# Kernel optimization log

Hardware: AMD Instinct MI355X
Metric: run time of the kernel (lower is better)

Reference implementation:

```python
import jax, jax.numpy as jnp
from jax import lax
import numpy as np

RADIUS = 0.05
N_SEEDS = 40

def _farthest_point_sample(xyz, npoint):
    # xyz: [B, N, 3] -> seed indices [B, npoint]
    B, N, _ = xyz.shape
    dist0 = jnp.full((B, N), 1e10, dtype=xyz.dtype)
    far0 = jnp.zeros((B,), dtype=jnp.int32)  # deterministic init (torch uses randint)
    batch_idx = jnp.arange(B)

    def step(carry, _):
        distance, farthest = carry
        centroid = xyz[batch_idx, farthest][:, None, :]          # [B,1,3]
        d = jnp.sum((xyz - centroid) ** 2, axis=-1)              # [B,N]
        distance = jnp.minimum(distance, d)
        new_far = jnp.argmax(distance, axis=-1).astype(jnp.int32)
        return (distance, new_far), farthest

    _, cents = lax.scan(step, (dist0, far0), None, length=npoint)
    return cents.T                                               # [B, npoint]

def setup_inputs() -> dict:
    key = jax.random.key(0)
    pcs = jax.random.uniform(key, (16, 65536, 3), dtype=jnp.float32)
    return {"pcs": pcs}

def reference(pcs) -> jnp.ndarray:
    B, N, C = pcs.shape
    S = N_SEEDS
    seeds = _farthest_point_sample(pcs, S)                       # [B,S] int
    new_xyz = pcs[jnp.arange(B)[:, None], seeds]                 # [B,S,3]
    # squared pairwise distances seeds->points: [B,S,N]
    sqrdists = (jnp.sum(new_xyz ** 2, -1)[:, :, None]
                + jnp.sum(pcs ** 2, -1)[:, None, :]
                - 2.0 * jnp.einsum('bsc,bnc->bsn', new_xyz, pcs))
    relu_dists = jax.nn.relu(RADIUS ** 2 - sqrdists)
    den_mat = jnp.sum(relu_dists, axis=2)                        # [B,S]
    den_var = jnp.var(den_mat, axis=1, ddof=1).mean()            # torch.var is unbiased
    return den_var
```

## Files before the change

kernel.cpp:

```cpp
#include <hip/hip_runtime.h>

typedef unsigned long long ull;

#define NB    16
#define NPTS  65536
#define NSEED 40
#define BPB   16
#define TPB   1024
#define NW    16
#define PPT   4
#define R2    0.0025f
#define PAYLOAD 0xFFFFFFFFFFFFull
#define DONEG 40ull

__device__ __forceinline__ ull packdi(float v, int idx) {
  return ((ull)__float_as_uint(v) << 16) | (ull)((unsigned)(idx ^ 0xFFFF) & 0xFFFFu);
}

__global__ __launch_bounds__(TPB, 4) void fps_den_kernel(
    const float* __restrict__ pcs, ull* __restrict__ slots,
    ull* __restrict__ pden, float* __restrict__ out)
{
  const int beta = blockIdx.x >> 4;
  const int blk  = blockIdx.x & 15;
  const int tid  = threadIdx.x;
  const int lane = tid & 63;
  const int wav  = tid >> 6;
  const float* __restrict__ base = pcs + (size_t)beta * (NPTS * 3);

  __shared__ ull   sRedP[2][NW];
  __shared__ float sRedX[2][NW], sRedY[2][NW], sRedZ[2][NW];
  __shared__ float sWx[2], sWy[2], sWz[2];
  __shared__ float sSx[NSEED], sSy[NSEED], sSz[NSEED];
  __shared__ float sDen[NW][NSEED];
  __shared__ float sV[NB];

  float px[PPT], py[PPT], pz[PPT], dist[PPT];
#pragma unroll
  for (int j = 0; j < PPT; ++j) {
    int n = blk * (TPB * PPT) + j * TPB + tid;
    px[j] = base[n * 3 + 0];
    py[j] = base[n * 3 + 1];
    pz[j] = base[n * 3 + 2];
    dist[j] = 1e10f;
  }

  float cx = base[0], cy = base[1], cz = base[2];
  if (tid == 0) { sSx[0] = cx; sSy[0] = cy; sSz[0] = cz; }

  ull* myslots = slots + (size_t)beta * (2 * BPB * 4);

  for (int k = 0; k < NSEED - 1; ++k) {
    ull bestp = 0; float bx = 0.f, by = 0.f, bz = 0.f;
#pragma unroll
    for (int j = 0; j < PPT; ++j) {
      float dx = px[j] - cx, dy = py[j] - cy, dz = pz[j] - cz;
      float d  = __fadd_rn(__fadd_rn(__fmul_rn(dx, dx), __fmul_rn(dy, dy)),
                           __fmul_rn(dz, dz));
      float nd = fminf(dist[j], d);
      dist[j]  = nd;
      int n    = blk * (TPB * PPT) + j * TPB + tid;
      ull p    = packdi(nd, n);
      if (p > bestp) { bestp = p; bx = px[j]; by = py[j]; bz = pz[j]; }
    }
    ull mx = bestp;
#pragma unroll
    for (int o = 32; o > 0; o >>= 1) {
      ull q = __shfl_xor(mx, o, 64);
      mx = mx > q ? mx : q;
    }
    ull bal = __ballot(bestp == mx);
    int src = __ffsll((long long)bal) - 1;
    float gx = __shfl(bx, src, 64);
    float gy = __shfl(by, src, 64);
    float gz = __shfl(bz, src, 64);
    if (lane == 0) {
      sRedP[k & 1][wav] = mx;
      sRedX[k & 1][wav] = gx; sRedY[k & 1][wav] = gy; sRedZ[k & 1][wav] = gz;
    }
    __syncthreads();

    const ull gen = (ull)(k + 1);
    const ull g48 = gen << 48;
    ull* arr = myslots + (size_t)((k + 1) & 1) * (BPB * 4);

    if (wav == 0) {
      ull rp = (lane < NW) ? sRedP[k & 1][lane] : 0;
      ull m2 = rp;
#pragma unroll
      for (int o = 8; o > 0; o >>= 1) {
        ull q = __shfl_xor(m2, o, 64);
        m2 = m2 > q ? m2 : q;
      }
      ull bal2 = __ballot((rp == m2) && (lane < NW));
      int s2 = __ffsll((long long)bal2) - 1;
      float rx = sRedX[k & 1][s2];
      float ry = sRedY[k & 1][s2];
      float rz = sRedZ[k & 1][s2];
      ull rec = g48 | (m2 & PAYLOAD);
      if (lane == 1) rec = g48 | (ull)__float_as_uint(rx);
      if (lane == 2) rec = g48 | (ull)__float_as_uint(ry);
      if (lane == 3) rec = g48 | (ull)__float_as_uint(rz);
      if (lane < 4)
        __hip_atomic_store(&arr[blk * 4 + lane], rec,
                           __ATOMIC_RELAXED, __HIP_MEMORY_SCOPE_AGENT);

      ull vcur = __hip_atomic_load(&arr[lane], __ATOMIC_RELAXED,
                                   __HIP_MEMORY_SCOPE_AGENT);
      for (;;) {
        ull vnext = __hip_atomic_load(&arr[lane], __ATOMIC_RELAXED,
                                      __HIP_MEMORY_SCOPE_AGENT);
        if (__all((int)((vcur >> 48) == gen))) break;
        vcur = vnext;
      }
      ull pl = ((lane & 3) == 0) ? (vcur & PAYLOAD) : 0;
      ull m = pl;
#pragma unroll
      for (int o = 32; o > 0; o >>= 1) {
        ull q = __shfl_xor(m, o, 64);
        m = m > q ? m : q;
      }
      ull balw = __ballot((pl == m) && ((lane & 3) == 0));
      int srcw = __ffsll((long long)balw) - 1;
      float f   = __uint_as_float((unsigned)(vcur & 0xFFFFFFFFull));
      float wx2 = __shfl(f, srcw + 1, 64);
      float wy2 = __shfl(f, srcw + 2, 64);
      float wz2 = __shfl(f, srcw + 3, 64);
      if (lane == 0) {
        sWx[k & 1] = wx2; sWy[k & 1] = wy2; sWz[k & 1] = wz2;
        sSx[k + 1] = wx2; sSy[k + 1] = wy2; sSz[k + 1] = wz2;
      }
    } else {
      float da = 0.f;
#pragma unroll
      for (int j = 0; j < PPT; ++j) {
        float dx = px[j] - cx, dy = py[j] - cy, dz = pz[j] - cz;
        float d  = dx * dx + dy * dy + dz * dz;
        da += fmaxf(R2 - d, 0.f);
      }
#pragma unroll
      for (int o = 32; o > 0; o >>= 1) da += __shfl_xor(da, o, 64);
      if (lane == 0) sDen[wav][k] = da;
    }
    __syncthreads();
    cx = sWx[k & 1]; cy = sWy[k & 1]; cz = sWz[k & 1];
  }

  if (wav == 0) {
    for (int s = 0; s < NSEED; ++s) {
      float sx = sSx[s], sy = sSy[s], sz = sSz[s];
      float a = 0.f;
#pragma unroll
      for (int j = 0; j < PPT; ++j) {
        float dx = px[j] - sx, dy = py[j] - sy, dz = pz[j] - sz;
        float d  = dx * dx + dy * dy + dz * dz;
        a += fmaxf(R2 - d, 0.f);
      }
#pragma unroll
      for (int o = 32; o > 0; o >>= 1) a += __shfl_xor(a, o, 64);
      if (lane == 0) sDen[0][s] = a;
    }
  } else {
    float a = 0.f;
#pragma unroll
    for (int j = 0; j < PPT; ++j) {
      float dx = px[j] - cx, dy = py[j] - cy, dz = pz[j] - cz;
      float d  = dx * dx + dy * dy + dz * dz;
      a += fmaxf(R2 - d, 0.f);
    }
#pragma unroll
    for (int o = 32; o > 0; o >>= 1) a += __shfl_xor(a, o, 64);
    if (lane == 0) sDen[wav][NSEED - 1] = a;
  }
  __syncthreads();

  if (tid < NSEED) {
    float t = 0.f;
#pragma unroll
    for (int w = 0; w < NW; ++w) t += sDen[w][tid];
    ull rec = (DONEG << 48) | (ull)__float_as_uint(t);
    __hip_atomic_store(&pden[((size_t)beta * BPB + blk) * NSEED + tid], rec,
                       __ATOMIC_RELAXED, __HIP_MEMORY_SCOPE_AGENT);
  }

  if (blockIdx.x == 0) {
    __syncthreads();
    if (tid < NB * NSEED) {
      int b0 = tid / NSEED, s = tid - b0 * NSEED;
      float a = 0.f;
#pragma unroll
      for (int c = 0; c < 2; ++c) {
        ull v[8];
#pragma unroll
        for (int b = 0; b < 8; ++b)
          v[b] = __hip_atomic_load(
              &pden[((size_t)b0 * BPB + c * 8 + b) * NSEED + s],
              __ATOMIC_RELAXED, __HIP_MEMORY_SCOPE_AGENT);
        for (;;) {
          bool ok = true;
#pragma unroll
          for (int b = 0; b < 8; ++b)
            if ((v[b] >> 48) != DONEG) {
              ok = false;
              v[b] = __hip_atomic_load(
                  &pden[((size_t)b0 * BPB + c * 8 + b) * NSEED + s],
                  __ATOMIC_RELAXED, __HIP_MEMORY_SCOPE_AGENT);
            }
          if (ok) break;
        }
#pragma unroll
        for (int b = 0; b < 8; ++b)
          a += __uint_as_float((unsigned)(v[b] & 0xFFFFFFFFull));
      }
      sDen[b0][s] = a;
    }
    __syncthreads();
    if (tid < NB) {
      float m = 0.f;
      for (int s = 0; s < NSEED; ++s) m += sDen[tid][s];
      m /= (float)NSEED;
      float q = 0.f;
      for (int s = 0; s < NSEED; ++s) { float d = sDen[tid][s] - m; q += d * d; }
      sV[tid] = q / (float)(NSEED - 1);
    }
    __syncthreads();
    if (tid == 0) {
      float v = 0.f;
      for (int i = 0; i < NB; ++i) v += sV[i];
      out[0] = v / (float)NB;
    }
  }
}

extern "C" void kernel_launch(void* const* d_in, const int* in_sizes, int n_in,
                              void* d_out, int out_size, void* d_ws, size_t ws_size,
                              hipStream_t stream) {
  const float* pcs = (const float*)d_in[0];
  float* out  = (float*)d_out;
  ull*   pden = (ull*)d_ws;
  ull*   slots = (ull*)((char*)d_ws + 81920);

  fps_den_kernel<<<dim3(NB * BPB), dim3(TPB), 0, stream>>>(pcs, slots, pden, out);
}
```

Before: 180.6 us.

## Batch multiple FPS seeds per cross-block sync round using top-4 candidates

Each block now publishes its top-4 packed (distance,index) candidates instead of only its maximum. After the cross-block exchange, wave 0 greedily accepts several seeds per round (up to MAXACC) for as long as it can show that the next FPS pick is among the known candidates. Per-seed density work is batched over the accepted seeds. The aim is fewer global grid-sync rounds across the 39 sequential FPS steps. The cost is extra shuffle reductions, per-candidate global loads of coordinates, and a more intricate correctness argument for the acceptance bound.

```diff
diff --git a/kernel.cpp b/kernel.cpp
--- a/kernel.cpp
+++ b/kernel.cpp
@@ -12,9 +12,19 @@
 #define R2    0.0025f
 #define PAYLOAD 0xFFFFFFFFFFFFull
 #define DONEG 40ull
+#define MAXACC 12
 
 __device__ __forceinline__ ull packdi(float v, int idx) {
   return ((ull)__float_as_uint(v) << 16) | (ull)((unsigned)(idx ^ 0xFFFF) & 0xFFFFu);
+}
+
+__device__ __forceinline__ ull bmax64(ull x) {
+#pragma unroll
+  for (int o = 32; o > 0; o >>= 1) {
+    ull q = __shfl_xor(x, o, 64);
+    x = x > q ? x : q;
+  }
+  return x;
 }
 
 __global__ __launch_bounds__(TPB, 4) void fps_den_kernel(
@@ -28,9 +38,9 @@
   const int wav  = tid >> 6;
   const float* __restrict__ base = pcs + (size_t)beta * (NPTS * 3);
 
-  __shared__ ull   sRedP[2][NW];
-  __shared__ float sRedX[2][NW], sRedY[2][NW], sRedZ[2][NW];
-  __shared__ float sWx[2], sWy[2], sWz[2];
+  __shared__ ull   sRedP[2][NW][4];
+  __shared__ float sWx[2][MAXACC], sWy[2][MAXACC], sWz[2][MAXACC];
+  __shared__ int   sWn[2];
   __shared__ float sSx[NSEED], sSy[NSEED], sSz[NSEED];
   __shared__ float sDen[NW][NSEED];
   __shared__ float sV[NB];
@@ -45,62 +55,77 @@
     dist[j] = 1e10f;
   }
 
-  float cx = base[0], cy = base[1], cz = base[2];
-  if (tid == 0) { sSx[0] = cx; sSy[0] = cy; sSz[0] = cz; }
+  if (tid == 0) {
+    float cx = base[0], cy = base[1], cz = base[2];
+    sSx[0] = cx; sSy[0] = cy; sSz[0] = cz;
+    sWx[0][0] = cx; sWy[0][0] = cy; sWz[0][0] = cz;
+  }
+  __syncthreads();
 
   ull* myslots = slots + (size_t)beta * (2 * BPB * 4);
 
-  for (int k = 0; k < NSEED - 1; ++k) {
-    ull bestp = 0; float bx = 0.f, by = 0.f, bz = 0.f;
+  int e = 0;
+  int sbase = 0;
+  int pcnt  = 1;
+  while (sbase + pcnt < NSEED) {
+    ++e;
+    const int pp  = (e - 1) & 1;
+    const int par = e & 1;
+
+    for (int i = 0; i < pcnt; ++i) {
+      const float cx = sWx[pp][i], cy = sWy[pp][i], cz = sWz[pp][i];
+#pragma unroll
+      for (int j = 0; j < PPT; ++j) {
+        float dx = px[j] - cx, dy = py[j] - cy, dz = pz[j] - cz;
+        float d  = __fadd_rn(__fadd_rn(__fmul_rn(dx, dx), __fmul_rn(dy, dy)),
+                             __fmul_rn(dz, dz));
+        dist[j] = fminf(dist[j], d);
+      }
+    }
+
+    ull kk[PPT];
 #pragma unroll
     for (int j = 0; j < PPT; ++j) {
-      float dx = px[j] - cx, dy = py[j] - cy, dz = pz[j] - cz;
-      float d  = __fadd_rn(__fadd_rn(__fmul_rn(dx, dx), __fmul_rn(dy, dy)),
-                           __fmul_rn(dz, dz));
-      float nd = fminf(dist[j], d);
-      dist[j]  = nd;
-      int n    = blk * (TPB * PPT) + j * TPB + tid;
-      ull p    = packdi(nd, n);
-      if (p > bestp) { bestp = p; bx = px[j]; by = py[j]; bz = pz[j]; }
-    }
-    ull mx = bestp;
-#pragma unroll
-    for (int o = 32; o > 0; o >>= 1) {
-      ull q = __shfl_xor(mx, o, 64);
-      mx = mx > q ? mx : q;
-    }
-    ull bal = __ballot(bestp == mx);
-    int src = __ffsll((long long)bal) - 1;
-    float gx = __shfl(bx, src, 64);
-    float gy = __shfl(by, src, 64);
-    float gz = __shfl(bz, src, 64);
+      int n = blk * (TPB * PPT) + j * TPB + tid;
+      kk[j] = packdi(dist[j], n);
+    }
+    ull s0, s1, s2, s3;
+    { ull b = 0;
+#pragma unroll
+      for (int j = 0; j < PPT; ++j) b = kk[j] > b ? kk[j] : b;
+      s0 = bmax64(b); }
+    { ull b = 0;
+#pragma unroll
+      for (int j = 0; j < PPT; ++j) { ull k = kk[j]; if (k != s0 && k > b) b = k; }
+      s1 = bmax64(b); }
+    { ull b = 0;
+#pragma unroll
+      for (int j = 0; j < PPT; ++j) { ull k = kk[j]; if (k != s0 && k != s1 && k > b) b = k; }
+      s2 = bmax64(b); }
+    { ull b = 0;
+#pragma unroll
+      for (int j = 0; j < PPT; ++j) { ull k = kk[j]; if (k != s0 && k != s1 && k != s2 && k > b) b = k; }
+      s3 = bmax64(b); }
     if (lane == 0) {
-      sRedP[k & 1][wav] = mx;
-      sRedX[k & 1][wav] = gx; sRedY[k & 1][wav] = gy; sRedZ[k & 1][wav] = gz;
-    }
-    __syncthreads();
-
-    const ull gen = (ull)(k + 1);
+      sRedP[par][wav][0] = s0; sRedP[par][wav][1] = s1;
+      sRedP[par][wav][2] = s2; sRedP[par][wav][3] = s3;
+    }
+    __syncthreads();
+
+    const ull gen = (ull)e;
     const ull g48 = gen << 48;
-    ull* arr = myslots + (size_t)((k + 1) & 1) * (BPB * 4);
+    ull* arr = myslots + (size_t)par * (BPB * 4);
 
     if (wav == 0) {
-      ull rp = (lane < NW) ? sRedP[k & 1][lane] : 0;
-      ull m2 = rp;
-#pragma unroll
-      for (int o = 8; o > 0; o >>= 1) {
-        ull q = __shfl_xor(m2, o, 64);
-        m2 = m2 > q ? m2 : q;
-      }
-      ull bal2 = __ballot((rp == m2) && (lane < NW));
-      int s2 = __ffsll((long long)bal2) - 1;
-      float rx = sRedX[k & 1][s2];
-      float ry = sRedY[k & 1][s2];
-      float rz = sRedZ[k & 1][s2];
-      ull rec = g48 | (m2 & PAYLOAD);
-      if (lane == 1) rec = g48 | (ull)__float_as_uint(rx);
-      if (lane == 2) rec = g48 | (ull)__float_as_uint(ry);
-      if (lane == 3) rec = g48 | (ull)__float_as_uint(rz);
+      ull c = sRedP[par][lane >> 2][lane & 3];
+      ull m0 = bmax64(c);
+      ull m1 = bmax64(c == m0 ? 0 : c);
+      ull m2 = bmax64((c == m0 || c == m1) ? 0 : c);
+      ull m3 = bmax64((c == m0 || c == m1 || c == m2) ? 0 : c);
+      ull rec = g48 | (m0 & PAYLOAD);
+      if (lane == 1) rec = g48 | (m1 & PAYLOAD);
+      if (lane == 2) rec = g48 | (m2 & PAYLOAD);
+      if (lane == 3) rec = g48 | (m3 & PAYLOAD);
       if (lane < 4)
         __hip_atomic_store(&arr[blk * 4 + lane], rec,
                            __ATOMIC_RELAXED, __HIP_MEMORY_SCOPE_AGENT);
@@ -113,37 +138,63 @@
         if (__all((int)((vcur >> 48) == gen))) break;
         vcur = vnext;
       }
-      ull pl = ((lane & 3) == 0) ? (vcur & PAYLOAD) : 0;
-      ull m = pl;
-#pragma unroll
-      for (int o = 32; o > 0; o >>= 1) {
-        ull q = __shfl_xor(m, o, 64);
-        m = m > q ? m : q;
-      }
-      ull balw = __ballot((pl == m) && ((lane & 3) == 0));
-      int srcw = __ffsll((long long)balw) - 1;
-      float f   = __uint_as_float((unsigned)(vcur & 0xFFFFFFFFull));
-      float wx2 = __shfl(f, srcw + 1, 64);
-      float wy2 = __shfl(f, srcw + 2, 64);
-      float wz2 = __shfl(f, srcw + 3, 64);
-      if (lane == 0) {
-        sWx[k & 1] = wx2; sWy[k & 1] = wy2; sWz[k & 1] = wz2;
-        sSx[k + 1] = wx2; sSy[k + 1] = wy2; sSz[k + 1] = wz2;
-      }
+      ull p = vcur & PAYLOAD;
+
+      ull F = bmax64(((lane & 3) == 3) ? p : 0);
+      bool alive = (p >= F);
+      float qx = 0.f, qy = 0.f, qz = 0.f;
+      if (alive) {
+        int idx = (int)((p ^ 0xFFFFull) & 0xFFFFull);
+        const float* q = base + 3 * idx;
+        qx = q[0]; qy = q[1]; qz = q[2];
+      }
+
+      ull ck = p;
+      int acc = 0;
+      int maxacc = NSEED - (sbase + pcnt);
+      if (maxacc > MAXACC) maxacc = MAXACC;
+      while (acc < maxacc) {
+        ull wk = bmax64(alive ? ck : 0);
+        if (wk < F) break;
+        ull bal = __ballot(alive && (ck == wk));
+        int src = __ffsll((long long)bal) - 1;
+        float wx = __shfl(qx, src, 64);
+        float wy = __shfl(qy, src, 64);
+        float wz = __shfl(qz, src, 64);
+        if (lane == 0) {
+          sWx[par][acc] = wx; sWy[par][acc] = wy; sWz[par][acc] = wz;
+          int sidx = sbase + pcnt + acc;
+          sSx[sidx] = wx; sSy[sidx] = wy; sSz[sidx] = wz;
+        }
+        if (lane == src) alive = false;
+        if (alive) {
+          float dx = qx - wx, dy = qy - wy, dz = qz - wz;
+          float d  = __fadd_rn(__fadd_rn(__fmul_rn(dx, dx), __fmul_rn(dy, dy)),
+                               __fmul_rn(dz, dz));
+          float cd = __uint_as_float((unsigned)(ck >> 16));
+          if (d < cd) ck = ((ull)__float_as_uint(d) << 16) | (ck & 0xFFFFull);
+        }
+        ++acc;
+      }
+      if (lane == 0) sWn[par] = acc;
     } else {
-      float da = 0.f;
-#pragma unroll
-      for (int j = 0; j < PPT; ++j) {
-        float dx = px[j] - cx, dy = py[j] - cy, dz = pz[j] - cz;
-        float d  = dx * dx + dy * dy + dz * dz;
-        da += fmaxf(R2 - d, 0.f);
-      }
-#pragma unroll
-      for (int o = 32; o > 0; o >>= 1) da += __shfl_xor(da, o, 64);
-      if (lane == 0) sDen[wav][k] = da;
-    }
-    __syncthreads();
-    cx = sWx[k & 1]; cy = sWy[k & 1]; cz = sWz[k & 1];
+      for (int i = 0; i < pcnt; ++i) {
+        const float cx = sWx[pp][i], cy = sWy[pp][i], cz = sWz[pp][i];
+        float da = 0.f;
+#pragma unroll
+        for (int j = 0; j < PPT; ++j) {
+          float dx = px[j] - cx, dy = py[j] - cy, dz = pz[j] - cz;
+          float d  = dx * dx + dy * dy + dz * dz;
+          da += fmaxf(R2 - d, 0.f);
+        }
+#pragma unroll
+        for (int o = 32; o > 0; o >>= 1) da += __shfl_xor(da, o, 64);
+        if (lane == 0) sDen[wav][sbase + i] = da;
+      }
+    }
+    __syncthreads();
+    sbase += pcnt;
+    pcnt = sWn[par];
   }
 
   if (wav == 0) {
@@ -161,16 +212,20 @@
       if (lane == 0) sDen[0][s] = a;
     }
   } else {
-    float a = 0.f;
-#pragma unroll
-    for (int j = 0; j < PPT; ++j) {
-      float dx = px[j] - cx, dy = py[j] - cy, dz = pz[j] - cz;
-      float d  = dx * dx + dy * dy + dz * dz;
-      a += fmaxf(R2 - d, 0.f);
-    }
-#pragma unroll
-    for (int o = 32; o > 0; o >>= 1) a += __shfl_xor(a, o, 64);
-    if (lane == 0) sDen[wav][NSEED - 1] = a;
+    const int fp = e & 1;
+    for (int i = 0; i < pcnt; ++i) {
+      const float cx = sWx[fp][i], cy = sWy[fp][i], cz = sWz[fp][i];
+      float a = 0.f;
+#pragma unroll
+      for (int j = 0; j < PPT; ++j) {
+        float dx = px[j] - cx, dy = py[j] - cy, dz = pz[j] - cz;
+        float d  = dx * dx + dy * dy + dz * dz;
+        a += fmaxf(R2 - d, 0.f);
+      }
+#pragma unroll
+      for (int o = 32; o > 0; o >>= 1) a += __shfl_xor(a, o, 64);
+      if (lane == 0) sDen[wav][sbase + i] = a;
+    }
   }
   __syncthreads();
 
@@ -239,6 +294,5 @@
   float* out  = (float*)d_out;
   ull*   pden = (ull*)d_ws;
   ull*   slots = (ull*)((char*)d_ws + 81920);
-
   fps_den_kernel<<<dim3(NB * BPB), dim3(TPB), 0, stream>>>(pcs, slots, pden, out);
 }
```

Measured after the change: 219.1 us. 21.3% more time.
